# Performance work log

Measured on AMD Instinct MI355X. Metric: run time of the kernel, lower is better.

The kernel has to match this reference:

```python
import jax, jax.numpy as jnp
import numpy as np

T, B, DICO, EMB, LAT = 256, 64, 8192, 256, 256


def setup_inputs() -> dict:
    key = jax.random.key(0)
    ks = jax.random.split(key, 7)
    s_emb = 1.0 / np.sqrt(DICO)
    s_enc = 1.0 / np.sqrt(EMB + LAT)
    return {
        "x": jax.random.normal(ks[0], (T, B, DICO), dtype=jnp.float32),
        "h": jax.random.normal(ks[1], (B, LAT), dtype=jnp.float32),
        "W_emb": jax.random.uniform(ks[2], (DICO, EMB), jnp.float32, -s_emb, s_emb),
        "b_emb": jax.random.uniform(ks[3], (EMB,), jnp.float32, -s_emb, s_emb),
        "W_enc": jax.random.uniform(ks[4], (EMB + LAT, LAT), jnp.float32, -s_enc, s_enc),
        "b_enc": jax.random.uniform(ks[5], (LAT,), jnp.float32, -s_enc, s_enc),
    }


def reference(x, h, W_emb, b_emb, W_enc, b_enc):
    # embedding: [T,B,DICO] @ [DICO,EMB] -> [T,B,EMB]
    xe = jnp.einsum('tbd,de->tbe', x, W_emb) + b_emb
    # split encoder weight into x-part and h-part: cat(x,h)@W == x@Wx + h@Wh
    Wx, Wh = W_enc[:EMB], W_enc[EMB:]
    # hoist the per-step x projection out of the scan (no h dependence)
    xp = jnp.einsum('tbe,el->tbl', xe, Wx) + b_enc  # [T,B,LAT]

    def step(h, xp_t):
        h_new = jnp.tanh(xp_t + h @ Wh)
        return h_new, h_new

    _, hs = jax.lax.scan(step, h, xp)
    return hs  # [T,B,LAT]
```

## Files before the change

kernel.cpp:

```cpp
#include <hip/hip_runtime.h>
#include <hip/hip_bf16.h>
#include <stdint.h>

#define T_DIM 256
#define B_DIM 64
#define DICO  8192
#define EMB   256
#define LAT   256
#define M_DIM (T_DIM*B_DIM)

#define BM 128
#define BN 256
#define BK 64
#define KSPLIT 2
#define KCHUNK (DICO/KSPLIT)
#define NKS (KCHUNK/BK)

typedef short  bf16x8 __attribute__((ext_vector_type(8)));
typedef float  f32x4  __attribute__((ext_vector_type(4)));
typedef _Float16 f16x2 __attribute__((ext_vector_type(2)));

__device__ __forceinline__ ushort f2bf(float f) {
  uint32_t u = __float_as_uint(f);
  u += 0x7FFFu + ((u >> 16) & 1u);
  return (ushort)(u >> 16);
}

__device__ __forceinline__ void glds16(const void* g, void* l) {
  __builtin_amdgcn_global_load_lds(
      (const __attribute__((address_space(1))) uint32_t*)g,
      (__attribute__((address_space(3))) uint32_t*)l, 16, 0, 0);
}

__global__ void wct_kernel(const float* __restrict__ Wemb, const float* __restrict__ Wenc,
                           ushort* __restrict__ wct) {
  const int n  = threadIdx.x;
  const int d0 = blockIdx.x * 32;
  __shared__ float we[32 * 256];
  __shared__ float tr[32 * 257];
  #pragma unroll
  for (int r = 0; r < 32; ++r) we[r*256 + n] = Wemb[(size_t)(d0 + r)*EMB + n];
  __syncthreads();
  float acc[32];
  #pragma unroll
  for (int d = 0; d < 32; ++d) acc[d] = 0.f;
  for (int e = 0; e < 256; ++e) {
    float wv = Wenc[e*LAT + n];
    #pragma unroll
    for (int d = 0; d < 32; ++d) acc[d] += we[d*256 + e] * wv;
  }
  #pragma unroll
  for (int d = 0; d < 32; ++d) tr[d*257 + n] = acc[d];
  __syncthreads();
  const int nn0 = n >> 2, kc = n & 3;
  #pragma unroll
  for (int p = 0; p < 4; ++p) {
    int nn = p*64 + nn0;
    bf16x8 v;
    #pragma unroll
    for (int j = 0; j < 8; ++j) v[j] = (short)f2bf(tr[(kc*8 + j)*257 + nn]);
    *(bf16x8*)(wct + (size_t)nn*DICO + d0 + kc*8) = v;
  }
}

__global__ void __launch_bounds__(256, 1) gemm_kernel(const float* __restrict__ x,
                                                      const ushort* __restrict__ wct,
                                                      float* __restrict__ xp) {
  __shared__ __align__(16) ushort sA[2][BM * BK];
  __shared__ __align__(16) ushort sB[2][BN * BK];
  const int tid = threadIdx.x;
  const int bid = blockIdx.x;
  const int swzb = (bid & 7) * 32 + (bid >> 3);
  const int mt = swzb & 127, ksp = swzb >> 7;
  const size_t rowbase = (size_t)mt * BM;
  const int kbase = ksp * KCHUNK;

  const int lane = tid & 63, wid = tid >> 6;
  const int l15 = lane & 15, lc = lane >> 4;

  const int r0 = tid >> 2, c0 = tid & 3;
  const float* ag0 = x + (rowbase + r0) * (size_t)DICO + kbase + c0 * 16;
  const float* ag1 = ag0 + (size_t)64 * DICO;
  const int aw0 = ((((r0      ) >> 4) * 2 + (c0 >> 1)) * 64 + (r0 & 15) + (c0 & 1) * 32) * 16;
  const int aw1 = ((((r0 + 64 ) >> 4) * 2 + (c0 >> 1)) * 64 + (r0 & 15) + (c0 & 1) * 32) * 16;

  const char* wb = (const char*)wct;
  const size_t kb2 = (size_t)kbase * 2;

  f32x4 acc[8][4];
  #pragma unroll
  for (int m = 0; m < 8; ++m)
    #pragma unroll
    for (int n = 0; n < 4; ++n) acc[m][n] = (f32x4){0.f, 0.f, 0.f, 0.f};

  float4 av[8];

  auto loadA = [&](int kofs) {
    #pragma unroll
    for (int q = 0; q < 4; ++q) av[q]     = *(const float4*)(ag0 + kofs + q * 4);
    #pragma unroll
    for (int q = 0; q < 4; ++q) av[4 + q] = *(const float4*)(ag1 + kofs + q * 4);
  };
  auto stageB = [&](int buf, int kofs) {
    #pragma unroll
    for (int r = 0; r < 8; ++r) {
      const int g = r * 4 + wid;
      const int srow  = (g >> 1) * 16 + l15;
      const int skoff = (g & 1) * 32 + lc * 8;
      glds16(wb + (size_t)srow * (DICO * 2) + kb2 + (size_t)(kofs + skoff) * 2,
             (char*)&sB[buf][0] + r * 4096 + tid * 16);
    }
  };
  auto storeA = [&](int buf) {
    #pragma unroll
    for (int h = 0; h < 2; ++h) {
      const float4 a0 = av[h*4+0], a1 = av[h*4+1], a2 = av[h*4+2], a3 = av[h*4+3];
      bf16x8 w0, w1;
      w0[0]=(short)f2bf(a0.x); w0[1]=(short)f2bf(a0.y); w0[2]=(short)f2bf(a0.z); w0[3]=(short)f2bf(a0.w);
      w0[4]=(short)f2bf(a1.x); w0[5]=(short)f2bf(a1.y); w0[6]=(short)f2bf(a1.z); w0[7]=(short)f2bf(a1.w);
      w1[0]=(short)f2bf(a2.x); w1[1]=(short)f2bf(a2.y); w1[2]=(short)f2bf(a2.z); w1[3]=(short)f2bf(a2.w);
      w1[4]=(short)f2bf(a3.x); w1[5]=(short)f2bf(a3.y); w1[6]=(short)f2bf(a3.z); w1[7]=(short)f2bf(a3.w);
      char* base = (char*)&sA[buf][0] + (h ? aw1 : aw0);
      *(bf16x8*)(base)       = w0;
      *(bf16x8*)(base + 256) = w1;
    }
  };
  auto compute = [&](int buf) {
    bf16x8 bfr[4][2];
    #pragma unroll
    for (int n = 0; n < 4; ++n)
      #pragma unroll
      for (int k2 = 0; k2 < 2; ++k2)
        bfr[n][k2] = *(const bf16x8*)((char*)&sB[buf][0] + ((((wid*4 + n)*2 + k2) * 64 + lane) * 16));
    #pragma unroll
    for (int m = 0; m < 8; ++m) {
      bf16x8 a0 = *(const bf16x8*)((char*)&sA[buf][0] + (((m*2 + 0) * 64 + lane) * 16));
      bf16x8 a1 = *(const bf16x8*)((char*)&sA[buf][0] + (((m*2 + 1) * 64 + lane) * 16));
      #pragma unroll
      for (int n = 0; n < 4; ++n) {
        acc[m][n] = __builtin_amdgcn_mfma_f32_16x16x32_bf16(a0, bfr[n][0], acc[m][n], 0, 0, 0);
        acc[m][n] = __builtin_amdgcn_mfma_f32_16x16x32_bf16(a1, bfr[n][1], acc[m][n], 0, 0, 0);
      }
    }
  };

  loadA(0);
  stageB(0, 0);
  storeA(0);
  __syncthreads();

  int cur = 0;
  for (int ks = 0; ks < NKS; ++ks) {
    const int kn = (ks + 1) * BK;
    if (ks + 1 < NKS) { loadA(kn); stageB(cur ^ 1, kn); }
    compute(cur);
    if (ks + 1 < NKS) storeA(cur ^ 1);
    __syncthreads();
    cur ^= 1;
  }

  float* xpo = xp + ((size_t)ksp * M_DIM + rowbase) * LAT;
  #pragma unroll
  for (int m = 0; m < 8; ++m)
    #pragma unroll
    for (int n = 0; n < 4; ++n)
      #pragma unroll
      for (int j = 0; j < 4; ++j)
        xpo[(size_t)(m*16 + lc*4 + j) * LAT + wid*64 + n*16 + l15] = acc[m][n][j];
}

__global__ void __launch_bounds__(256, 1) rnn_kernel(const float* __restrict__ xp,
                           const float* __restrict__ h0, const float* __restrict__ Wenc,
                           const float* __restrict__ bemb, const float* __restrict__ benc,
                           float* __restrict__ out) {
  const int b = blockIdx.x, l = threadIdx.x;
  __shared__ __align__(16) uint32_t hbuf[2][128];
  float bc = benc[l];
  #pragma unroll 8
  for (int e = 0; e < 256; ++e) bc += bemb[e] * Wenc[e*LAT + l];
  f16x2 wh[128];
  #pragma unroll
  for (int j = 0; j < 128; ++j) {
    f16x2 w;
    w[0] = (_Float16)Wenc[(size_t)(EMB + 2*j    )*LAT + l];
    w[1] = (_Float16)Wenc[(size_t)(EMB + 2*j + 1)*LAT + l];
    wh[j] = w;
  }
  ((_Float16*)&hbuf[0][0])[l] = (_Float16)h0[(size_t)b*LAT + l];
  __syncthreads();
  const float* xpb = xp + (size_t)b*LAT + l;
  float*       ob  = out + (size_t)b*LAT + l;
  const size_t ST = (size_t)B_DIM * LAT;
  const size_t PO = (size_t)M_DIM * LAT;
  float xa0 = xpb[0],  xa1 = xpb[PO];
  float xb0 = xpb[ST], xb1 = xpb[ST + PO];
  float xc0 = 0.f, xc1 = 0.f;
  for (int t = 0; t < T_DIM; ++t) {
    if (t + 2 < T_DIM) {
      size_t ni = (size_t)(t + 2) * ST;
      xc0 = xpb[ni]; xc1 = xpb[ni + PO];
    }
    const uint32_t* hc = &hbuf[t & 1][0];
    float s0=0.f,s1=0.f,s2=0.f,s3=0.f,s4=0.f,s5=0.f,s6=0.f,s7=0.f;
    #pragma unroll
    for (int q = 0; q < 16; ++q) {
      uint4 hv0 = *(const uint4*)(hc + q*8);
      uint4 hv1 = *(const uint4*)(hc + q*8 + 4);
      s0 = __builtin_amdgcn_fdot2(wh[q*8+0], __builtin_bit_cast(f16x2, hv0.x), s0, false);
      s1 = __builtin_amdgcn_fdot2(wh[q*8+1], __builtin_bit_cast(f16x2, hv0.y), s1, false);
      s2 = __builtin_amdgcn_fdot2(wh[q*8+2], __builtin_bit_cast(f16x2, hv0.z), s2, false);
      s3 = __builtin_amdgcn_fdot2(wh[q*8+3], __builtin_bit_cast(f16x2, hv0.w), s3, false);
      s4 = __builtin_amdgcn_fdot2(wh[q*8+4], __builtin_bit_cast(f16x2, hv1.x), s4, false);
      s5 = __builtin_amdgcn_fdot2(wh[q*8+5], __builtin_bit_cast(f16x2, hv1.y), s5, false);
      s6 = __builtin_amdgcn_fdot2(wh[q*8+6], __builtin_bit_cast(f16x2, hv1.z), s6, false);
      s7 = __builtin_amdgcn_fdot2(wh[q*8+7], __builtin_bit_cast(f16x2, hv1.w), s7, false);
    }
    float pre = (xa0 + xa1) + bc + (((s0+s1)+(s2+s3)) + ((s4+s5)+(s6+s7)));
    float ax = fabsf(pre);
    float e2 = __expf(-2.f * ax);
    float r  = __fdividef(1.f - e2, 1.f + e2);
    float hn = (pre < 0.f) ? -r : r;
    ob[(size_t)t * ST] = hn;
    ((_Float16*)&hbuf[(t + 1) & 1][0])[l] = (_Float16)hn;
    __builtin_amdgcn_sched_barrier(0);
    asm volatile("s_waitcnt lgkmcnt(0)" ::: "memory");
    __builtin_amdgcn_s_barrier();
    __builtin_amdgcn_sched_barrier(0);
    xa0 = xb0; xa1 = xb1; xb0 = xc0; xb1 = xc1;
  }
}

extern "C" void kernel_launch(void* const* d_in, const int* in_sizes, int n_in,
                              void* d_out, int out_size, void* d_ws, size_t ws_size,
                              hipStream_t stream) {
  const float* x    = (const float*)d_in[0];
  const float* h0   = (const float*)d_in[1];
  const float* Wemb = (const float*)d_in[2];
  const float* bemb = (const float*)d_in[3];
  const float* Wenc = (const float*)d_in[4];
  const float* benc = (const float*)d_in[5];
  float* out = (float*)d_out;

  ushort* wct = (ushort*)d_ws;
  float*  xp  = (float*)((char*)d_ws + ((size_t)4 << 20));

  wct_kernel<<<256, 256, 0, stream>>>(Wemb, Wenc, wct);
  gemm_kernel<<<256, 256, 0, stream>>>(x, wct, xp);
  rnn_kernel<<<64, 256, 0, stream>>>(xp, h0, Wenc, bemb, benc, out);
}
```

Baseline: 587.7 us.

## Split RNN recurrence dot product across four waves and swizzle GEMM LDS layout

The RNN kernel now uses 1024 threads per batch row. Each quarter computes a partial h@Wh dot product over 64 inputs, and the partials are reduced through shared memory before the tanh. The goal is to shorten the per-step serial dependency chain, at the cost of a second block barrier every step. The GEMM switches its A and B LDS tiles to row-major with XOR swizzling to reduce bank conflicts on loads, and an unroll pragma is added to the weight-combination loop.

```diff
diff --git a/kernel.cpp b/kernel.cpp
--- a/kernel.cpp
+++ b/kernel.cpp
@@ -44,6 +44,7 @@
   float acc[32];
   #pragma unroll
   for (int d = 0; d < 32; ++d) acc[d] = 0.f;
+  #pragma unroll 4
   for (int e = 0; e < 256; ++e) {
     float wv = Wenc[e*LAT + n];
     #pragma unroll
@@ -81,12 +82,18 @@
   const int r0 = tid >> 2, c0 = tid & 3;
   const float* ag0 = x + (rowbase + r0) * (size_t)DICO + kbase + c0 * 16;
   const float* ag1 = ag0 + (size_t)64 * DICO;
-  const int aw0 = ((((r0      ) >> 4) * 2 + (c0 >> 1)) * 64 + (r0 & 15) + (c0 & 1) * 32) * 16;
-  const int aw1 = ((((r0 + 64 ) >> 4) * 2 + (c0 >> 1)) * 64 + (r0 & 15) + (c0 & 1) * 32) * 16;
+  const int sx0 = (((2*c0    ) ^ (r0 & 7)) * 16);
+  const int sx1 = (((2*c0 + 1) ^ (r0 & 7)) * 16);
+
+  const int sw0 = (((    lc) ^ (l15 & 7)) * 16);
+  const int sw1 = (((4 + lc) ^ (l15 & 7)) * 16);
 
   const char* wb = (const char*)wct;
   const size_t kb2 = (size_t)kbase * 2;
 
+  const int brow_s = (tid >> 3);
+  const int bslot_s = tid & 7;
+
   f32x4 acc[8][4];
   #pragma unroll
   for (int m = 0; m < 8; ++m)
@@ -104,10 +111,9 @@
   auto stageB = [&](int buf, int kofs) {
     #pragma unroll
     for (int r = 0; r < 8; ++r) {
-      const int g = r * 4 + wid;
-      const int srow  = (g >> 1) * 16 + l15;
-      const int skoff = (g & 1) * 32 + lc * 8;
-      glds16(wb + (size_t)srow * (DICO * 2) + kb2 + (size_t)(kofs + skoff) * 2,
+      const int row = r * 32 + brow_s;
+      const int srcslot = bslot_s ^ (row & 7);
+      glds16(wb + (size_t)row * (DICO * 2) + kb2 + (size_t)kofs * 2 + srcslot * 16,
              (char*)&sB[buf][0] + r * 4096 + tid * 16);
     }
   };
@@ -120,22 +126,24 @@
       w0[4]=(short)f2bf(a1.x); w0[5]=(short)f2bf(a1.y); w0[6]=(short)f2bf(a1.z); w0[7]=(short)f2bf(a1.w);
       w1[0]=(short)f2bf(a2.x); w1[1]=(short)f2bf(a2.y); w1[2]=(short)f2bf(a2.z); w1[3]=(short)f2bf(a2.w);
       w1[4]=(short)f2bf(a3.x); w1[5]=(short)f2bf(a3.y); w1[6]=(short)f2bf(a3.z); w1[7]=(short)f2bf(a3.w);
-      char* base = (char*)&sA[buf][0] + (h ? aw1 : aw0);
-      *(bf16x8*)(base)       = w0;
-      *(bf16x8*)(base + 256) = w1;
+      char* base = (char*)&sA[buf][0] + (h ? (r0 + 64) : r0) * 128;
+      *(bf16x8*)(base + sx0) = w0;
+      *(bf16x8*)(base + sx1) = w1;
     }
   };
   auto compute = [&](int buf) {
     bf16x8 bfr[4][2];
     #pragma unroll
-    for (int n = 0; n < 4; ++n)
-      #pragma unroll
-      for (int k2 = 0; k2 < 2; ++k2)
-        bfr[n][k2] = *(const bf16x8*)((char*)&sB[buf][0] + ((((wid*4 + n)*2 + k2) * 64 + lane) * 16));
+    for (int n = 0; n < 4; ++n) {
+      const char* bb = (const char*)&sB[buf][0] + (wid*64 + n*16 + l15) * 128;
+      bfr[n][0] = *(const bf16x8*)(bb + sw0);
+      bfr[n][1] = *(const bf16x8*)(bb + sw1);
+    }
     #pragma unroll
     for (int m = 0; m < 8; ++m) {
-      bf16x8 a0 = *(const bf16x8*)((char*)&sA[buf][0] + (((m*2 + 0) * 64 + lane) * 16));
-      bf16x8 a1 = *(const bf16x8*)((char*)&sA[buf][0] + (((m*2 + 1) * 64 + lane) * 16));
+      const char* ab = (const char*)&sA[buf][0] + (m*16 + l15) * 128;
+      bf16x8 a0 = *(const bf16x8*)(ab + sw0);
+      bf16x8 a1 = *(const bf16x8*)(ab + sw1);
       #pragma unroll
       for (int n = 0; n < 4; ++n) {
         acc[m][n] = __builtin_amdgcn_mfma_f32_16x16x32_bf16(a0, bfr[n][0], acc[m][n], 0, 0, 0);
@@ -169,59 +177,79 @@
         xpo[(size_t)(m*16 + lc*4 + j) * LAT + wid*64 + n*16 + l15] = acc[m][n][j];
 }
 
-__global__ void __launch_bounds__(256, 1) rnn_kernel(const float* __restrict__ xp,
+__global__ void __launch_bounds__(1024, 4) rnn_kernel(const float* __restrict__ xp,
                            const float* __restrict__ h0, const float* __restrict__ Wenc,
                            const float* __restrict__ bemb, const float* __restrict__ benc,
                            float* __restrict__ out) {
-  const int b = blockIdx.x, l = threadIdx.x;
+  const int b = blockIdx.x;
+  const int tid = threadIdx.x;
+  const int q = tid >> 8;
+  const int l = tid & 255;
   __shared__ __align__(16) uint32_t hbuf[2][128];
-  float bc = benc[l];
-  #pragma unroll 8
-  for (int e = 0; e < 256; ++e) bc += bemb[e] * Wenc[e*LAT + l];
-  f16x2 wh[128];
-  #pragma unroll
-  for (int j = 0; j < 128; ++j) {
+  __shared__ __align__(16) float part[4][256];
+
+  f16x2 wh[32];
+  #pragma unroll
+  for (int j = 0; j < 32; ++j) {
     f16x2 w;
-    w[0] = (_Float16)Wenc[(size_t)(EMB + 2*j    )*LAT + l];
-    w[1] = (_Float16)Wenc[(size_t)(EMB + 2*j + 1)*LAT + l];
+    w[0] = (_Float16)Wenc[(size_t)(EMB + 64*q + 2*j    )*LAT + l];
+    w[1] = (_Float16)Wenc[(size_t)(EMB + 64*q + 2*j + 1)*LAT + l];
     wh[j] = w;
   }
-  ((_Float16*)&hbuf[0][0])[l] = (_Float16)h0[(size_t)b*LAT + l];
-  __syncthreads();
+  float bc = 0.f;
+  if (q == 0) {
+    bc = benc[l];
+    #pragma unroll 4
+    for (int e = 0; e < 256; ++e) bc += bemb[e] * Wenc[e*LAT + l];
+  }
+  if (tid < 128) {
+    f16x2 hp;
+    hp[0] = (_Float16)h0[(size_t)b*LAT + 2*tid];
+    hp[1] = (_Float16)h0[(size_t)b*LAT + 2*tid + 1];
+    hbuf[0][tid] = __builtin_bit_cast(uint32_t, hp);
+  }
+  __syncthreads();
+
   const float* xpb = xp + (size_t)b*LAT + l;
   float*       ob  = out + (size_t)b*LAT + l;
   const size_t ST = (size_t)B_DIM * LAT;
   const size_t PO = (size_t)M_DIM * LAT;
-  float xa0 = xpb[0],  xa1 = xpb[PO];
-  float xb0 = xpb[ST], xb1 = xpb[ST + PO];
-  float xc0 = 0.f, xc1 = 0.f;
+  float xa0 = 0.f, xa1 = 0.f, xb0 = 0.f, xb1 = 0.f, xc0 = 0.f, xc1 = 0.f;
+  if (q == 0) {
+    xa0 = xpb[0];  xa1 = xpb[PO];
+    xb0 = xpb[ST]; xb1 = xpb[ST + PO];
+  }
+
   for (int t = 0; t < T_DIM; ++t) {
-    if (t + 2 < T_DIM) {
+    if (q == 0 && t + 2 < T_DIM) {
       size_t ni = (size_t)(t + 2) * ST;
       xc0 = xpb[ni]; xc1 = xpb[ni + PO];
     }
-    const uint32_t* hc = &hbuf[t & 1][0];
-    float s0=0.f,s1=0.f,s2=0.f,s3=0.f,s4=0.f,s5=0.f,s6=0.f,s7=0.f;
-    #pragma unroll
-    for (int q = 0; q < 16; ++q) {
-      uint4 hv0 = *(const uint4*)(hc + q*8);
-      uint4 hv1 = *(const uint4*)(hc + q*8 + 4);
-      s0 = __builtin_amdgcn_fdot2(wh[q*8+0], __builtin_bit_cast(f16x2, hv0.x), s0, false);
-      s1 = __builtin_amdgcn_fdot2(wh[q*8+1], __builtin_bit_cast(f16x2, hv0.y), s1, false);
-      s2 = __builtin_amdgcn_fdot2(wh[q*8+2], __builtin_bit_cast(f16x2, hv0.z), s2, false);
-      s3 = __builtin_amdgcn_fdot2(wh[q*8+3], __builtin_bit_cast(f16x2, hv0.w), s3, false);
-      s4 = __builtin_amdgcn_fdot2(wh[q*8+4], __builtin_bit_cast(f16x2, hv1.x), s4, false);
-      s5 = __builtin_amdgcn_fdot2(wh[q*8+5], __builtin_bit_cast(f16x2, hv1.y), s5, false);
-      s6 = __builtin_amdgcn_fdot2(wh[q*8+6], __builtin_bit_cast(f16x2, hv1.z), s6, false);
-      s7 = __builtin_amdgcn_fdot2(wh[q*8+7], __builtin_bit_cast(f16x2, hv1.w), s7, false);
-    }
-    float pre = (xa0 + xa1) + bc + (((s0+s1)+(s2+s3)) + ((s4+s5)+(s6+s7)));
-    float ax = fabsf(pre);
-    float e2 = __expf(-2.f * ax);
-    float r  = __fdividef(1.f - e2, 1.f + e2);
-    float hn = (pre < 0.f) ? -r : r;
-    ob[(size_t)t * ST] = hn;
-    ((_Float16*)&hbuf[(t + 1) & 1][0])[l] = (_Float16)hn;
+    const uint32_t* hc = &hbuf[t & 1][q * 32];
+    float s0 = 0.f, s1 = 0.f, s2 = 0.f, s3 = 0.f;
+    #pragma unroll
+    for (int j = 0; j < 8; ++j) {
+      uint4 hv = *(const uint4*)(hc + j*4);
+      s0 = __builtin_amdgcn_fdot2(wh[j*4+0], __builtin_bit_cast(f16x2, hv.x), s0, false);
+      s1 = __builtin_amdgcn_fdot2(wh[j*4+1], __builtin_bit_cast(f16x2, hv.y), s1, false);
+      s2 = __builtin_amdgcn_fdot2(wh[j*4+2], __builtin_bit_cast(f16x2, hv.z), s2, false);
+      s3 = __builtin_amdgcn_fdot2(wh[j*4+3], __builtin_bit_cast(f16x2, hv.w), s3, false);
+    }
+    float p = (s0 + s1) + (s2 + s3);
+    part[q][l] = p;
+    __builtin_amdgcn_sched_barrier(0);
+    asm volatile("s_waitcnt lgkmcnt(0)" ::: "memory");
+    __builtin_amdgcn_s_barrier();
+    __builtin_amdgcn_sched_barrier(0);
+    if (q == 0) {
+      float pre = (xa0 + xa1) + bc + ((p + part[1][l]) + (part[2][l] + part[3][l]));
+      float ax = fabsf(pre);
+      float e2 = __expf(-2.f * ax);
+      float r  = __fdividef(1.f - e2, 1.f + e2);
+      float hn = (pre < 0.f) ? -r : r;
+      ob[(size_t)t * ST] = hn;
+      ((_Float16*)&hbuf[(t + 1) & 1][0])[l] = (_Float16)hn;
+    }
     __builtin_amdgcn_sched_barrier(0);
     asm volatile("s_waitcnt lgkmcnt(0)" ::: "memory");
     __builtin_amdgcn_s_barrier();
@@ -246,5 +274,5 @@
 
   wct_kernel<<<256, 256, 0, stream>>>(Wemb, Wenc, wct);
   gemm_kernel<<<256, 256, 0, stream>>>(x, wct, xp);
-  rnn_kernel<<<64, 256, 0, stream>>>(xp, h0, Wenc, bemb, benc, out);
-}
+  rnn_kernel<<<64, 1024, 0, stream>>>(xp, h0, Wenc, bemb, benc, out);
+}
```

Measured after the change: 649.2 us. 10.5% more time.

## Use 512-thread GEMM blocks with 2x4 warp grid and XOR-swizzled LDS layout

Applied to the files above, without the earlier changes.

The GEMM block doubles from 4 to 8 waves, arranged as a 2x4 grid, so each wave now computes a 64x64 sub-tile instead of 128x64. This halves per-thread accumulators and per-thread A loads and spreads the global-load and conversion work over more threads. The shared memory layout for A and B moves to row-major 128-byte rows with an XOR swizzle to avoid bank conflicts. The wct kernel's inner loop also gets unroll 4. More waves per CU can hide latency better, at the cost of more synchronization participants and possibly more LDS read traffic per MFMA.

```diff
diff --git a/kernel.cpp b/kernel.cpp
--- a/kernel.cpp
+++ b/kernel.cpp
@@ -44,6 +44,7 @@
   float acc[32];
   #pragma unroll
   for (int d = 0; d < 32; ++d) acc[d] = 0.f;
+  #pragma unroll 4
   for (int e = 0; e < 256; ++e) {
     float wv = Wenc[e*LAT + n];
     #pragma unroll
@@ -63,7 +64,7 @@
   }
 }
 
-__global__ void __launch_bounds__(256, 1) gemm_kernel(const float* __restrict__ x,
+__global__ void __launch_bounds__(512, 1) gemm_kernel(const float* __restrict__ x,
                                                       const ushort* __restrict__ wct,
                                                       float* __restrict__ xp) {
   __shared__ __align__(16) ushort sA[2][BM * BK];
@@ -77,65 +78,67 @@
 
   const int lane = tid & 63, wid = tid >> 6;
   const int l15 = lane & 15, lc = lane >> 4;
+  const int wr = wid >> 2, wc = wid & 3;
 
   const int r0 = tid >> 2, c0 = tid & 3;
-  const float* ag0 = x + (rowbase + r0) * (size_t)DICO + kbase + c0 * 16;
-  const float* ag1 = ag0 + (size_t)64 * DICO;
-  const int aw0 = ((((r0      ) >> 4) * 2 + (c0 >> 1)) * 64 + (r0 & 15) + (c0 & 1) * 32) * 16;
-  const int aw1 = ((((r0 + 64 ) >> 4) * 2 + (c0 >> 1)) * 64 + (r0 & 15) + (c0 & 1) * 32) * 16;
+  const float* ag = x + (rowbase + r0) * (size_t)DICO + kbase + c0 * 16;
+  const int sx0 = (((2*c0    ) ^ (r0 & 7)) * 16);
+  const int sx1 = (((2*c0 + 1) ^ (r0 & 7)) * 16);
+
+  const int sw0 = (((    lc) ^ (l15 & 7)) * 16);
+  const int sw1 = (((4 + lc) ^ (l15 & 7)) * 16);
 
   const char* wb = (const char*)wct;
   const size_t kb2 = (size_t)kbase * 2;
 
-  f32x4 acc[8][4];
-  #pragma unroll
-  for (int m = 0; m < 8; ++m)
+  const int brow_s = (tid >> 3);
+  const int bslot_s = tid & 7;
+
+  f32x4 acc[4][4];
+  #pragma unroll
+  for (int m = 0; m < 4; ++m)
     #pragma unroll
     for (int n = 0; n < 4; ++n) acc[m][n] = (f32x4){0.f, 0.f, 0.f, 0.f};
 
-  float4 av[8];
+  float4 av[4];
 
   auto loadA = [&](int kofs) {
     #pragma unroll
-    for (int q = 0; q < 4; ++q) av[q]     = *(const float4*)(ag0 + kofs + q * 4);
-    #pragma unroll
-    for (int q = 0; q < 4; ++q) av[4 + q] = *(const float4*)(ag1 + kofs + q * 4);
+    for (int q = 0; q < 4; ++q) av[q] = *(const float4*)(ag + kofs + q * 4);
   };
   auto stageB = [&](int buf, int kofs) {
     #pragma unroll
-    for (int r = 0; r < 8; ++r) {
-      const int g = r * 4 + wid;
-      const int srow  = (g >> 1) * 16 + l15;
-      const int skoff = (g & 1) * 32 + lc * 8;
-      glds16(wb + (size_t)srow * (DICO * 2) + kb2 + (size_t)(kofs + skoff) * 2,
-             (char*)&sB[buf][0] + r * 4096 + tid * 16);
+    for (int r = 0; r < 4; ++r) {
+      const int row = r * 64 + brow_s;
+      const int srcslot = bslot_s ^ (row & 7);
+      glds16(wb + (size_t)row * (DICO * 2) + kb2 + (size_t)kofs * 2 + srcslot * 16,
+             (char*)&sB[buf][0] + r * 8192 + tid * 16);
     }
   };
   auto storeA = [&](int buf) {
-    #pragma unroll
-    for (int h = 0; h < 2; ++h) {
-      const float4 a0 = av[h*4+0], a1 = av[h*4+1], a2 = av[h*4+2], a3 = av[h*4+3];
-      bf16x8 w0, w1;
-      w0[0]=(short)f2bf(a0.x); w0[1]=(short)f2bf(a0.y); w0[2]=(short)f2bf(a0.z); w0[3]=(short)f2bf(a0.w);
-      w0[4]=(short)f2bf(a1.x); w0[5]=(short)f2bf(a1.y); w0[6]=(short)f2bf(a1.z); w0[7]=(short)f2bf(a1.w);
-      w1[0]=(short)f2bf(a2.x); w1[1]=(short)f2bf(a2.y); w1[2]=(short)f2bf(a2.z); w1[3]=(short)f2bf(a2.w);
-      w1[4]=(short)f2bf(a3.x); w1[5]=(short)f2bf(a3.y); w1[6]=(short)f2bf(a3.z); w1[7]=(short)f2bf(a3.w);
-      char* base = (char*)&sA[buf][0] + (h ? aw1 : aw0);
-      *(bf16x8*)(base)       = w0;
-      *(bf16x8*)(base + 256) = w1;
-    }
+    const float4 a0 = av[0], a1 = av[1], a2 = av[2], a3 = av[3];
+    bf16x8 w0, w1;
+    w0[0]=(short)f2bf(a0.x); w0[1]=(short)f2bf(a0.y); w0[2]=(short)f2bf(a0.z); w0[3]=(short)f2bf(a0.w);
+    w0[4]=(short)f2bf(a1.x); w0[5]=(short)f2bf(a1.y); w0[6]=(short)f2bf(a1.z); w0[7]=(short)f2bf(a1.w);
+    w1[0]=(short)f2bf(a2.x); w1[1]=(short)f2bf(a2.y); w1[2]=(short)f2bf(a2.z); w1[3]=(short)f2bf(a2.w);
+    w1[4]=(short)f2bf(a3.x); w1[5]=(short)f2bf(a3.y); w1[6]=(short)f2bf(a3.z); w1[7]=(short)f2bf(a3.w);
+    char* base = (char*)&sA[buf][0] + r0 * 128;
+    *(bf16x8*)(base + sx0) = w0;
+    *(bf16x8*)(base + sx1) = w1;
   };
   auto compute = [&](int buf) {
     bf16x8 bfr[4][2];
     #pragma unroll
-    for (int n = 0; n < 4; ++n)
-      #pragma unroll
-      for (int k2 = 0; k2 < 2; ++k2)
-        bfr[n][k2] = *(const bf16x8*)((char*)&sB[buf][0] + ((((wid*4 + n)*2 + k2) * 64 + lane) * 16));
-    #pragma unroll
-    for (int m = 0; m < 8; ++m) {
-      bf16x8 a0 = *(const bf16x8*)((char*)&sA[buf][0] + (((m*2 + 0) * 64 + lane) * 16));
-      bf16x8 a1 = *(const bf16x8*)((char*)&sA[buf][0] + (((m*2 + 1) * 64 + lane) * 16));
+    for (int n = 0; n < 4; ++n) {
+      const char* bb = (const char*)&sB[buf][0] + (wc*64 + n*16 + l15) * 128;
+      bfr[n][0] = *(const bf16x8*)(bb + sw0);
+      bfr[n][1] = *(const bf16x8*)(bb + sw1);
+    }
+    #pragma unroll
+    for (int m = 0; m < 4; ++m) {
+      const char* ab = (const char*)&sA[buf][0] + (wr*64 + m*16 + l15) * 128;
+      bf16x8 a0 = *(const bf16x8*)(ab + sw0);
+      bf16x8 a1 = *(const bf16x8*)(ab + sw1);
       #pragma unroll
       for (int n = 0; n < 4; ++n) {
         acc[m][n] = __builtin_amdgcn_mfma_f32_16x16x32_bf16(a0, bfr[n][0], acc[m][n], 0, 0, 0);
@@ -161,12 +164,12 @@
 
   float* xpo = xp + ((size_t)ksp * M_DIM + rowbase) * LAT;
   #pragma unroll
-  for (int m = 0; m < 8; ++m)
+  for (int m = 0; m < 4; ++m)
     #pragma unroll
     for (int n = 0; n < 4; ++n)
       #pragma unroll
       for (int j = 0; j < 4; ++j)
-        xpo[(size_t)(m*16 + lc*4 + j) * LAT + wid*64 + n*16 + l15] = acc[m][n][j];
+        xpo[(size_t)(wr*64 + m*16 + lc*4 + j) * LAT + wc*64 + n*16 + l15] = acc[m][n][j];
 }
 
 __global__ void __launch_bounds__(256, 1) rnn_kernel(const float* __restrict__ xp,
@@ -245,6 +248,6 @@
   float*  xp  = (float*)((char*)d_ws + ((size_t)4 << 20));
 
   wct_kernel<<<256, 256, 0, stream>>>(Wemb, Wenc, wct);
-  gemm_kernel<<<256, 256, 0, stream>>>(x, wct, xp);
+  gemm_kernel<<<256, 512, 0, stream>>>(x, wct, xp);
   rnn_kernel<<<64, 256, 0, stream>>>(xp, h0, Wenc, bemb, benc, out);
 }
```

Measured after the change: 673.2 us. +14.5%, slower.
